# Performance work log

Measured on AMD Instinct MI355X. Metric: run time of the kernel, lower is better.

## Reference

```python
import jax, jax.numpy as jnp
import numpy as np

H = 12        # num_heads
HD = 64       # head_dim
D = H * HD    # hidden_size = 768
N = 4096      # number of patches (64x64 grid)
SCALE = HD ** -0.5


def _rotate_half(x):
    half = x.shape[-1] // 2
    x1, x2 = x[..., :half], x[..., half:]
    return jnp.concatenate([-x2, x1], axis=-1)


def setup_inputs() -> dict:
    key = jax.random.key(0)
    ks = jax.random.split(key, 7)
    return {
        "hidden_states": jax.random.normal(ks[0], (N, D), jnp.float32),
        "cos": jax.random.uniform(ks[1], (N, HD), jnp.float32),
        "sin": jax.random.uniform(ks[2], (N, HD), jnp.float32),
        "qkv_w": jax.random.normal(ks[3], (D, 3 * D), jnp.float32) * (D ** -0.5),
        "qkv_b": jax.random.normal(ks[4], (3 * D,), jnp.float32) * 0.02,
        "proj_w": jax.random.normal(ks[5], (D, D), jnp.float32) * (D ** -0.5),
        "proj_b": jax.random.normal(ks[6], (D,), jnp.float32) * 0.02,
    }


def reference(hidden_states, cos, sin, qkv_w, qkv_b, proj_w, proj_b):
    n = hidden_states.shape[0]
    # fused QKV projection: (N, 3D) -> (N, 3, H, HD)
    qkv = (hidden_states @ qkv_w + qkv_b).reshape(n, 3, H, HD)
    q, k, v = qkv[:, 0], qkv[:, 1], qkv[:, 2]  # each (N, H, HD)

    # 2-D RoPE (HF apply_rotary_pos_emb_vision): cos/sin broadcast over heads
    c = cos[:, None, :]
    s = sin[:, None, :]
    q = q * c + _rotate_half(q) * s
    k = k * c + _rotate_half(k) * s

    # full bidirectional attention, heads-first layout
    q = q.transpose(1, 0, 2) * SCALE  # (H, N, HD)
    k = k.transpose(1, 0, 2)
    v = v.transpose(1, 0, 2)
    attn = jnp.einsum('hnd,hmd->hnm', q, k)      # (H, N, N)
    attn = jax.nn.softmax(attn, axis=-1)
    out = jnp.einsum('hnm,hmd->hnd', attn, v)    # (H, N, HD)
    out = out.transpose(1, 0, 2).reshape(n, D)
    return out @ proj_w + proj_b
```

## Files before the change

kernel.cpp:

```cpp
#include <hip/hip_runtime.h>
#include <stdint.h>

#define NTOK 4096
#define NH 12
#define HDIM 64
#define DMODEL 768
#define D3 2304

typedef __attribute__((ext_vector_type(8))) __bf16 bf16x8;
typedef __attribute__((ext_vector_type(4))) float f32x4;
typedef __attribute__((ext_vector_type(4))) unsigned int u32x4;

#define MFMA(a, b, c) __builtin_amdgcn_mfma_f32_16x16x32_bf16((a), (b), (c), 0, 0, 0)

__device__ __forceinline__ uint16_t f2bf(float f) {
  uint32_t u = __builtin_bit_cast(uint32_t, f) + 0x8000u;
  return (uint16_t)(u >> 16);
}
__device__ __forceinline__ uint32_t packrd(float a, float b) {
  uint32_t ua = __builtin_bit_cast(uint32_t, a) + 0x8000u;
  uint32_t ub = __builtin_bit_cast(uint32_t, b) + 0x8000u;
  return __builtin_amdgcn_perm(ub, ua, 0x07060302u);
}
__device__ __forceinline__ float bf2f(uint16_t u) {
  uint32_t v = ((uint32_t)u) << 16;
  return __builtin_bit_cast(float, v);
}
__device__ __forceinline__ void gld_lds16(const uint16_t* g, uint16_t* l) {
  __builtin_amdgcn_global_load_lds((const __attribute__((address_space(1))) void*)g,
                                   (__attribute__((address_space(3))) void*)l, 16, 0, 0);
}

__global__ void va_cast_bf16(const float* __restrict__ in, uint16_t* __restrict__ out, int n4) {
  int i = blockIdx.x * 256 + threadIdx.x;
  if (i >= n4) return;
  float4 v = ((const float4*)in)[i];
  ((uint2*)out)[i] = make_uint2(packrd(v.x, v.y), packrd(v.z, v.w));
}

__global__ void va_transpose_cast(const float* __restrict__ W, uint16_t* __restrict__ Wt,
                                  int K, int Ncols) {
  __shared__ uint16_t tile[32][36];
  const int t = threadIdx.x;
  const int k0 = blockIdx.y * 32, n0 = blockIdx.x * 32;
  {
    int i = t >> 3, j = (t & 7) * 4;
    float4 v = *(const float4*)(W + (size_t)(k0 + i) * Ncols + n0 + j);
    tile[i][j + 0] = f2bf(v.x);
    tile[i][j + 1] = f2bf(v.y);
    tile[i][j + 2] = f2bf(v.z);
    tile[i][j + 3] = f2bf(v.w);
  }
  __syncthreads();
  {
    int c = t >> 3, kk = (t & 7) * 4;
    uint32_t lo = (uint32_t)tile[kk + 0][c] | ((uint32_t)tile[kk + 1][c] << 16);
    uint32_t hi = (uint32_t)tile[kk + 2][c] | ((uint32_t)tile[kk + 3][c] << 16);
    *(uint2*)(Wt + (size_t)(n0 + c) * K + k0 + kk) = make_uint2(lo, hi);
  }
}

template <int MT, int OUT_BF16>
__global__ __launch_bounds__(256) void va_gemm97(const uint16_t* __restrict__ A,
                                                 const uint16_t* __restrict__ Bt,
                                                 const float* __restrict__ bias, void* Cout,
                                                 int M, int Nc, int K) {
  constexpr int NJ = (MT == 128) ? 4 : 2;
  __shared__ uint16_t As[MT * 32];
  __shared__ uint16_t Bs[128 * 32];
  const int t = threadIdx.x;
  const int w = t >> 6, ln = t & 63, quad = ln >> 4, l15 = ln & 15;
  const int m0 = blockIdx.y * MT, n0 = blockIdx.x * 128;
  const int wm = (MT == 128) ? (w & 1) * 64 : 0;
  const int wn = (MT == 128) ? (w >> 1) * 64 : w * 32;
  const int srow = t >> 2, scol = (t & 3) * 8;
  f32x4 acc[4][NJ] = {};
  for (int kk = 0; kk < K; kk += 32) {
#pragma unroll
    for (int p = 0; p < MT / 64; ++p)
      gld_lds16(A + (size_t)(m0 + p * 64 + srow) * K + kk + scol, As + (p * 64 + w * 16) * 32);
#pragma unroll
    for (int p = 0; p < 2; ++p)
      gld_lds16(Bt + (size_t)(n0 + p * 64 + srow) * K + kk + scol, Bs + (p * 64 + w * 16) * 32);
    __syncthreads();
    bf16x8 af[4], bfr[NJ];
#pragma unroll
    for (int i = 0; i < 4; ++i) af[i] = *(const bf16x8*)(As + (wm + i * 16 + l15) * 32 + quad * 8);
#pragma unroll
    for (int j = 0; j < NJ; ++j)
      bfr[j] = *(const bf16x8*)(Bs + (wn + j * 16 + l15) * 32 + quad * 8);
#pragma unroll
    for (int i = 0; i < 4; ++i)
#pragma unroll
      for (int j = 0; j < NJ; ++j) acc[i][j] = MFMA(af[i], bfr[j], acc[i][j]);
    __syncthreads();
  }
#pragma unroll
  for (int i = 0; i < 4; ++i) {
    int row = m0 + wm + i * 16 + quad * 4;
#pragma unroll
    for (int j = 0; j < NJ; ++j) {
      int col = n0 + wn + j * 16 + l15;
      float b = bias[col];
      if (OUT_BF16) {
        uint16_t* C = (uint16_t*)Cout;
#pragma unroll
        for (int rg = 0; rg < 4; ++rg) C[(size_t)(row + rg) * Nc + col] = f2bf(acc[i][j][rg] + b);
      } else {
        float* C = (float*)Cout;
#pragma unroll
        for (int rg = 0; rg < 4; ++rg) C[(size_t)(row + rg) * Nc + col] = acc[i][j][rg] + b;
      }
    }
  }
}

__global__ void va_rope_split(const uint16_t* __restrict__ qkvb, const float* __restrict__ cosb,
                              const float* __restrict__ sinb, uint16_t* __restrict__ Qg,
                              uint16_t* __restrict__ Kg, uint16_t* __restrict__ Vtg) {
  const int h = blockIdx.y;
  const int lane = threadIdx.x & 63;
  const int c = threadIdx.x >> 6;
  const int n = blockIdx.x * 64 + lane;
  const uint16_t* base = qkvb + (size_t)n * D3 + h * HDIM;
  const float QS = 0.125f * 1.4426950408889634f;
  float c0[8], s0[8], c1[8], s1[8];
  *(float4*)(c0) = *(const float4*)(cosb + (size_t)n * HDIM + c * 8);
  *(float4*)(c0 + 4) = *(const float4*)(cosb + (size_t)n * HDIM + c * 8 + 4);
  *(float4*)(s0) = *(const float4*)(sinb + (size_t)n * HDIM + c * 8);
  *(float4*)(s0 + 4) = *(const float4*)(sinb + (size_t)n * HDIM + c * 8 + 4);
  *(float4*)(c1) = *(const float4*)(cosb + (size_t)n * HDIM + c * 8 + 32);
  *(float4*)(c1 + 4) = *(const float4*)(cosb + (size_t)n * HDIM + c * 8 + 36);
  *(float4*)(s1) = *(const float4*)(sinb + (size_t)n * HDIM + c * 8 + 32);
  *(float4*)(s1 + 4) = *(const float4*)(sinb + (size_t)n * HDIM + c * 8 + 36);
#pragma unroll
  for (int mtx = 0; mtx < 2; ++mtx) {
    const uint16_t* src = base + mtx * DMODEL;
    uint16_t* dst = (mtx ? Kg : Qg) + ((size_t)h * NTOK + n) * HDIM;
    const float sc = mtx ? 1.0f : QS;
    uint16_t lo[8], hi[8];
    *(uint4*)lo = *(const uint4*)(src + c * 8);
    *(uint4*)hi = *(const uint4*)(src + c * 8 + 32);
    uint32_t outlo[4], outhi[4];
#pragma unroll
    for (int j = 0; j < 8; j += 2) {
      float x0 = bf2f(lo[j]), x1 = bf2f(lo[j + 1]);
      float y0 = bf2f(hi[j]), y1 = bf2f(hi[j + 1]);
      float a0 = (x0 * c0[j] - y0 * s0[j]) * sc;
      float a1 = (x1 * c0[j + 1] - y1 * s0[j + 1]) * sc;
      float b0 = (y0 * c1[j] + x0 * s1[j]) * sc;
      float b1 = (y1 * c1[j + 1] + x1 * s1[j + 1]) * sc;
      outlo[j >> 1] = packrd(a0, a1);
      outhi[j >> 1] = packrd(b0, b1);
    }
    *(uint4*)(dst + c * 8) = *(uint4*)outlo;
    *(uint4*)(dst + c * 8 + 32) = *(uint4*)outhi;
  }
  const int pl = (lane < 32) ? ((lane >> 2) * 8 + (lane & 3))
                             : (((lane - 32) >> 2) * 8 + 4 + (lane & 3));
  const int np = blockIdx.x * 64 + pl;
  uint16_t vv[16];
  *(uint4*)(vv) = *(const uint4*)(base + 2 * DMODEL + c * 16);
  *(uint4*)(vv + 8) = *(const uint4*)(base + 2 * DMODEL + c * 16 + 8);
#pragma unroll
  for (int j = 0; j < 16; ++j)
    Vtg[((size_t)h * HDIM + c * 16 + j) * NTOK + np] = vv[j];
}

__global__ __launch_bounds__(256, 3) void va_flash7(const uint16_t* __restrict__ Qg,
                                                    const uint16_t* __restrict__ Kg,
                                                    const uint16_t* __restrict__ Vtg,
                                                    uint16_t* __restrict__ Opb,
                                                    float* __restrict__ Lp) {
  __shared__ uint16_t Ks[2][2][64 * 32];
  __shared__ uint16_t Vs[2][64 * 64];
  const int t = threadIdx.x;
  const int w = t >> 6, ln = t & 63, quad = ln >> 4, l15 = ln & 15;
  const int h = blockIdx.y;
  const int qb = blockIdx.x & 31, ks = blockIdx.x >> 5;
  const int q0 = qb * 128, key0 = ks * 2048;

  bf16x8 qf[2][2];
#pragma unroll
  for (int s = 0; s < 2; ++s)
#pragma unroll
    for (int c = 0; c < 2; ++c)
      qf[s][c] = *(const bf16x8*)(Qg + ((size_t)h * NTOK + q0 + w * 32 + s * 16 + l15) * HDIM +
                                  c * 32 + quad * 8);
  f32x4 o[2][4] = {};
  float lpart[2] = {0.f, 0.f};
  const uint16_t* Kst =
      Kg + ((size_t)h * NTOK + key0 + w * 16 + (ln >> 2)) * HDIM + (ln & 3) * 8;
  const uint16_t* Vst =
      Vtg + ((size_t)h * HDIM + w * 16 + (ln >> 3)) * NTOK + key0 + (ln & 7) * 8;

  gld_lds16(Kst, &Ks[0][0][w * 16 * 32]);
  gld_lds16(Kst + 32, &Ks[0][1][w * 16 * 32]);
  gld_lds16(Vst, &Vs[0][w * 16 * 64]);
  gld_lds16(Vst + (size_t)8 * NTOK, &Vs[0][(w * 16 + 8) * 64]);

  for (int kt = 0; kt < 32; ++kt) {
    __syncthreads();
    const int cur = kt & 1;
    if (kt < 31) {
      const uint16_t* kb = Kst + (size_t)((kt + 1) * 64) * HDIM;
      gld_lds16(kb, &Ks[cur ^ 1][0][w * 16 * 32]);
      gld_lds16(kb + 32, &Ks[cur ^ 1][1][w * 16 * 32]);
      const uint16_t* vb = Vst + (kt + 1) * 64;
      gld_lds16(vb, &Vs[cur ^ 1][w * 16 * 64]);
      gld_lds16(vb + (size_t)8 * NTOK, &Vs[cur ^ 1][(w * 16 + 8) * 64]);
    }
    f32x4 st[2][4];
#pragma unroll
    for (int mt = 0; mt < 4; ++mt) {
      bf16x8 ka0 = *(const bf16x8*)(&Ks[cur][0][(mt * 16 + l15) * 32 + quad * 8]);
      bf16x8 ka1 = *(const bf16x8*)(&Ks[cur][1][(mt * 16 + l15) * 32 + quad * 8]);
#pragma unroll
      for (int s = 0; s < 2; ++s) {
        f32x4 z = {};
        z = MFMA(ka0, qf[s][0], z);
        st[s][mt] = MFMA(ka1, qf[s][1], z);
      }
    }
    bf16x8 vf[4][2];
#pragma unroll
    for (int dt = 0; dt < 4; ++dt)
#pragma unroll
      for (int H = 0; H < 2; ++H)
        vf[dt][H] = *(const bf16x8*)(&Vs[cur][(dt * 16 + l15) * 64 + H * 32 + quad * 8]);
#pragma unroll
    for (int s = 0; s < 2; ++s) {
      uint32_t Ppk[4][2];
      float ls = 0.f;
#pragma unroll
      for (int mt = 0; mt < 4; ++mt) {
        float p0 = __builtin_amdgcn_exp2f(st[s][mt][0]);
        float p1 = __builtin_amdgcn_exp2f(st[s][mt][1]);
        float p2 = __builtin_amdgcn_exp2f(st[s][mt][2]);
        float p3 = __builtin_amdgcn_exp2f(st[s][mt][3]);
        ls += (p0 + p1) + (p2 + p3);
        Ppk[mt][0] = packrd(p0, p1);
        Ppk[mt][1] = packrd(p2, p3);
      }
      lpart[s] += ls;
#pragma unroll
      for (int H = 0; H < 2; ++H) {
        u32x4 d = {Ppk[H][0], Ppk[H][1], Ppk[H + 2][0], Ppk[H + 2][1]};
        bf16x8 pf = __builtin_bit_cast(bf16x8, d);
#pragma unroll
        for (int dt = 0; dt < 4; ++dt) o[s][dt] = MFMA(vf[dt][H], pf, o[s][dt]);
      }
    }
  }
  uint16_t* ob = Opb + ((size_t)(ks * NH + h) * HDIM) * NTOK;
#pragma unroll
  for (int s = 0; s < 2; ++s) {
    int q = q0 + w * 32 + s * 16 + l15;
    float l = lpart[s];
    l += __shfl_xor(l, 16, 64);
    l += __shfl_xor(l, 32, 64);
#pragma unroll
    for (int dt = 0; dt < 4; ++dt)
#pragma unroll
      for (int rg = 0; rg < 4; ++rg)
        ob[(size_t)(dt * 16 + quad * 4 + rg) * NTOK + q] = f2bf(o[s][dt][rg]);
    if (quad == 0) Lp[(size_t)(ks * NH + h) * NTOK + q] = l;
  }
}

__global__ __launch_bounds__(256) void va_combine2(const uint16_t* __restrict__ Opb,
                                                   const float* __restrict__ Lp,
                                                   uint16_t* __restrict__ Ob) {
  __shared__ uint16_t T[64][72];
  const int h = blockIdx.y;
  const int n0 = blockIdx.x * 64;
  const int t = threadIdx.x;
  const int lane = t & 63, c = t >> 6;
  const int n = n0 + lane;
  float lsum = Lp[(size_t)h * NTOK + n] + Lp[(size_t)(NH + h) * NTOK + n];
  const float inv = 1.0f / lsum;
#pragma unroll
  for (int j = 0; j < 16; j += 2) {
    int d = c * 16 + j;
    float r0 = 0.f, r1 = 0.f;
#pragma unroll
    for (int s = 0; s < 2; ++s) {
      const uint16_t* p = Opb + ((size_t)(s * NH + h) * HDIM + d) * NTOK + n;
      r0 += bf2f(p[0]);
      r1 += bf2f(p[NTOK]);
    }
    *(uint32_t*)(&T[lane][d]) = packrd(r0 * inv, r1 * inv);
  }
  __syncthreads();
  const int row = t >> 2, ch = t & 3;
  uint4 a = *(const uint4*)(&T[row][ch * 16]);
  uint4 b = *(const uint4*)(&T[row][ch * 16 + 8]);
  uint16_t* dst = Ob + (size_t)(n0 + row) * DMODEL + h * HDIM + ch * 16;
  *(uint4*)dst = a;
  *(uint4*)(dst + 8) = b;
}

extern "C" void kernel_launch(void* const* d_in, const int* in_sizes, int n_in, void* d_out,
                              int out_size, void* d_ws, size_t ws_size, hipStream_t stream) {
  (void)in_sizes; (void)n_in; (void)out_size; (void)ws_size;
  const float* hidden = (const float*)d_in[0];
  const float* cosb = (const float*)d_in[1];
  const float* sinb = (const float*)d_in[2];
  const float* qkv_w = (const float*)d_in[3];
  const float* qkv_b = (const float*)d_in[4];
  const float* proj_w = (const float*)d_in[5];
  const float* proj_b = (const float*)d_in[6];
  float* out = (float*)d_out;

  char* ws = (char*)d_ws;
  size_t off = 0;
  auto alloc = [&](size_t bytes) {
    void* p = ws + off;
    off += (bytes + 255) & ~(size_t)255;
    return p;
  };
  uint16_t* Abf = (uint16_t*)alloc((size_t)NTOK * DMODEL * 2);
  uint16_t* Wqt = (uint16_t*)alloc((size_t)D3 * DMODEL * 2);
  uint16_t* Wpt = (uint16_t*)alloc((size_t)DMODEL * DMODEL * 2);
  uint16_t* qkvb = (uint16_t*)alloc((size_t)NTOK * D3 * 2);
  uint16_t* Qb = (uint16_t*)alloc((size_t)NH * NTOK * HDIM * 2);
  uint16_t* Kb = (uint16_t*)alloc((size_t)NH * NTOK * HDIM * 2);
  uint16_t* Vtb = (uint16_t*)alloc((size_t)NH * NTOK * HDIM * 2);
  uint16_t* Ob = (uint16_t*)alloc((size_t)NTOK * DMODEL * 2);
  uint16_t* Opb = (uint16_t*)alloc((size_t)2 * NH * HDIM * NTOK * 2);
  float* Lp = (float*)alloc((size_t)2 * NH * NTOK * 4);

  va_cast_bf16<<<(NTOK * DMODEL / 4 + 255) / 256, 256, 0, stream>>>(hidden, Abf,
                                                                    NTOK * DMODEL / 4);
  va_transpose_cast<<<dim3(D3 / 32, DMODEL / 32), 256, 0, stream>>>(qkv_w, Wqt, DMODEL, D3);
  va_transpose_cast<<<dim3(DMODEL / 32, DMODEL / 32), 256, 0, stream>>>(proj_w, Wpt, DMODEL,
                                                                        DMODEL);
  va_gemm97<128, 1><<<dim3(D3 / 128, NTOK / 128), 256, 0, stream>>>(Abf, Wqt, qkv_b, qkvb, NTOK,
                                                                    D3, DMODEL);
  va_rope_split<<<dim3(NTOK / 64, NH), 256, 0, stream>>>(qkvb, cosb, sinb, Qb, Kb, Vtb);
  va_flash7<<<dim3(64, NH), 256, 0, stream>>>(Qb, Kb, Vtb, Opb, Lp);
  va_combine2<<<dim3(NTOK / 64, NH), 256, 0, stream>>>(Opb, Lp, Ob);
  va_gemm97<64, 0><<<dim3(DMODEL / 128, NTOK / 64), 256, 0, stream>>>(Ob, Wpt, proj_b, out, NTOK,
                                                                      DMODEL, DMODEL);
}
```

Before: 210.9 us.

## Split transposed V into two half-planes to match K-style LDS loads

The rope/split kernel now writes the transposed V into two separate planes, each holding half of every 64-key tile (32 keys per row, 2048 columns per plane). This lets the flash kernel load V tiles into LDS with the same 32-wide row pattern used for K, and it replaces recomputed per-iteration addresses with incremented pointers. The aim is more contiguous global-to-LDS transfers and cheaper address arithmetic. The cost is more complex indexing in the V-permute write, which must stay consistent with the MFMA operand layout.

```diff
diff --git a/kernel.cpp b/kernel.cpp
--- a/kernel.cpp
+++ b/kernel.cpp
@@ -156,24 +156,24 @@
     *(uint4*)(dst + c * 8) = *(uint4*)outlo;
     *(uint4*)(dst + c * 8 + 32) = *(uint4*)outhi;
   }
-  const int pl = (lane < 32) ? ((lane >> 2) * 8 + (lane & 3))
-                             : (((lane - 32) >> 2) * 8 + 4 + (lane & 3));
-  const int np = blockIdx.x * 64 + pl;
+  const int H = (lane >> 4) & 1;
+  const int pos = ((lane >> 2) & 3) * 8 + ((lane >> 5) & 1) * 4 + (lane & 3);
+  const int col = blockIdx.x * 32 + pos;
   uint16_t vv[16];
   *(uint4*)(vv) = *(const uint4*)(base + 2 * DMODEL + c * 16);
   *(uint4*)(vv + 8) = *(const uint4*)(base + 2 * DMODEL + c * 16 + 8);
 #pragma unroll
   for (int j = 0; j < 16; ++j)
-    Vtg[((size_t)h * HDIM + c * 16 + j) * NTOK + np] = vv[j];
-}
-
-__global__ __launch_bounds__(256, 3) void va_flash7(const uint16_t* __restrict__ Qg,
+    Vtg[(((size_t)H * NH + h) * HDIM + c * 16 + j) * 2048 + col] = vv[j];
+}
+
+__global__ __launch_bounds__(256, 3) void va_flash8(const uint16_t* __restrict__ Qg,
                                                     const uint16_t* __restrict__ Kg,
                                                     const uint16_t* __restrict__ Vtg,
                                                     uint16_t* __restrict__ Opb,
                                                     float* __restrict__ Lp) {
   __shared__ uint16_t Ks[2][2][64 * 32];
-  __shared__ uint16_t Vs[2][64 * 64];
+  __shared__ uint16_t Vs[2][2][64 * 32];
   const int t = threadIdx.x;
   const int w = t >> 6, ln = t & 63, quad = ln >> 4, l15 = ln & 15;
   const int h = blockIdx.y;
@@ -191,24 +191,27 @@
   float lpart[2] = {0.f, 0.f};
   const uint16_t* Kst =
       Kg + ((size_t)h * NTOK + key0 + w * 16 + (ln >> 2)) * HDIM + (ln & 3) * 8;
-  const uint16_t* Vst =
-      Vtg + ((size_t)h * HDIM + w * 16 + (ln >> 3)) * NTOK + key0 + (ln & 7) * 8;
+  const uint16_t* Vst0 =
+      Vtg + (((size_t)0 * NH + h) * HDIM + w * 16 + (ln >> 2)) * 2048 + ks * 1024 + (ln & 3) * 8;
+  const uint16_t* Vst1 =
+      Vtg + (((size_t)1 * NH + h) * HDIM + w * 16 + (ln >> 2)) * 2048 + ks * 1024 + (ln & 3) * 8;
 
   gld_lds16(Kst, &Ks[0][0][w * 16 * 32]);
   gld_lds16(Kst + 32, &Ks[0][1][w * 16 * 32]);
-  gld_lds16(Vst, &Vs[0][w * 16 * 64]);
-  gld_lds16(Vst + (size_t)8 * NTOK, &Vs[0][(w * 16 + 8) * 64]);
+  gld_lds16(Vst0, &Vs[0][0][w * 16 * 32]);
+  gld_lds16(Vst1, &Vs[0][1][w * 16 * 32]);
 
   for (int kt = 0; kt < 32; ++kt) {
     __syncthreads();
     const int cur = kt & 1;
     if (kt < 31) {
-      const uint16_t* kb = Kst + (size_t)((kt + 1) * 64) * HDIM;
-      gld_lds16(kb, &Ks[cur ^ 1][0][w * 16 * 32]);
-      gld_lds16(kb + 32, &Ks[cur ^ 1][1][w * 16 * 32]);
-      const uint16_t* vb = Vst + (kt + 1) * 64;
-      gld_lds16(vb, &Vs[cur ^ 1][w * 16 * 64]);
-      gld_lds16(vb + (size_t)8 * NTOK, &Vs[cur ^ 1][(w * 16 + 8) * 64]);
+      Kst += 64 * HDIM;
+      Vst0 += 32;
+      Vst1 += 32;
+      gld_lds16(Kst, &Ks[cur ^ 1][0][w * 16 * 32]);
+      gld_lds16(Kst + 32, &Ks[cur ^ 1][1][w * 16 * 32]);
+      gld_lds16(Vst0, &Vs[cur ^ 1][0][w * 16 * 32]);
+      gld_lds16(Vst1, &Vs[cur ^ 1][1][w * 16 * 32]);
     }
     f32x4 st[2][4];
 #pragma unroll
@@ -227,7 +230,7 @@
     for (int dt = 0; dt < 4; ++dt)
 #pragma unroll
       for (int H = 0; H < 2; ++H)
-        vf[dt][H] = *(const bf16x8*)(&Vs[cur][(dt * 16 + l15) * 64 + H * 32 + quad * 8]);
+        vf[dt][H] = *(const bf16x8*)(&Vs[cur][H][(dt * 16 + l15) * 32 + quad * 8]);
 #pragma unroll
     for (int s = 0; s < 2; ++s) {
       uint32_t Ppk[4][2];
@@ -325,7 +328,7 @@
   uint16_t* qkvb = (uint16_t*)alloc((size_t)NTOK * D3 * 2);
   uint16_t* Qb = (uint16_t*)alloc((size_t)NH * NTOK * HDIM * 2);
   uint16_t* Kb = (uint16_t*)alloc((size_t)NH * NTOK * HDIM * 2);
-  uint16_t* Vtb = (uint16_t*)alloc((size_t)NH * NTOK * HDIM * 2);
+  uint16_t* Vtb = (uint16_t*)alloc((size_t)2 * NH * HDIM * 2048 * 2);
   uint16_t* Ob = (uint16_t*)alloc((size_t)NTOK * DMODEL * 2);
   uint16_t* Opb = (uint16_t*)alloc((size_t)2 * NH * HDIM * NTOK * 2);
   float* Lp = (float*)alloc((size_t)2 * NH * NTOK * 4);
@@ -338,7 +341,7 @@
   va_gemm97<128, 1><<<dim3(D3 / 128, NTOK / 128), 256, 0, stream>>>(Abf, Wqt, qkv_b, qkvb, NTOK,
                                                                     D3, DMODEL);
   va_rope_split<<<dim3(NTOK / 64, NH), 256, 0, stream>>>(qkvb, cosb, sinb, Qb, Kb, Vtb);
-  va_flash7<<<dim3(64, NH), 256, 0, stream>>>(Qb, Kb, Vtb, Opb, Lp);
+  va_flash8<<<dim3(64, NH), 256, 0, stream>>>(Qb, Kb, Vtb, Opb, Lp);
   va_combine2<<<dim3(NTOK / 64, NH), 256, 0, stream>>>(Opb, Lp, Ob);
   va_gemm97<64, 0><<<dim3(DMODEL / 128, NTOK / 64), 256, 0, stream>>>(Ob, Wpt, proj_b, out, NTOK,
                                                                       DMODEL, DMODEL);
```

Measured after the change: 210.6 us. No clear change (-0.2%).
